# Performance work log

Measured on AMD Instinct MI355X. Metric: run time of the kernel, lower is better.

Reference implementation:

```python
import jax, jax.numpy as jnp
import numpy as np

C = 768; NH = 12; HD = C // NH; P = 16; IMG = 256; HS = IMG // P  # 16x16 patch grid
WIN = 7; HWP = WIN // 2  # half window (pad)
DEPTH = 12; MLP = 4 * C
B = 32; T = 1
OFFS = [(dh, dw) for dh in range(WIN) for dw in range(WIN)]


def ln(x, g, b, eps=1e-5):
    mu = jnp.mean(x, axis=-1, keepdims=True)
    var = jnp.mean((x - mu) ** 2, axis=-1, keepdims=True)
    return (x - mu) * jax.lax.rsqrt(var + eps) * g + b


def local_attn(x, qkv_w, proj_w, proj_b):
    # x: (B, N, C) with N = HS*HS (T=1); sliding-window attention, zero-padded keys
    Bc, N, _ = x.shape
    qkv = (x @ qkv_w.T).reshape(Bc, N, 3, NH, HD)
    q, k, v = [jnp.transpose(qkv[:, :, i], (0, 2, 1, 3)).reshape(Bc, NH, HS, HS, HD)
               for i in range(3)]
    scale = HD ** -0.5
    kp = jnp.pad(k, ((0, 0), (0, 0), (HWP, HWP), (HWP, HWP), (0, 0)))
    vp = jnp.pad(v, ((0, 0), (0, 0), (HWP, HWP), (HWP, HWP), (0, 0)))
    # per-offset logits; padded (zero) keys give logit 0, matching torch's zero-pad softmax
    scores = jnp.stack([
        jnp.einsum('bnhwd,bnhwd->bnhw', q, kp[:, :, dh:dh + HS, dw:dw + HS]) * scale
        for dh, dw in OFFS], axis=-1)  # (B, NH, HS, HS, 49)
    attn = jax.nn.softmax(scores, axis=-1)
    out = sum(attn[..., i, None] * vp[:, :, dh:dh + HS, dw:dw + HS]
              for i, (dh, dw) in enumerate(OFFS))  # (B, NH, HS, HS, HD)
    out = jnp.transpose(out, (0, 2, 3, 1, 4)).reshape(Bc, N, C)
    return out @ proj_w.T + proj_b


def global_attn(x, in_w, in_b, out_w, out_b):
    Bc, N, _ = x.shape
    qkv = x @ in_w.T + in_b
    q, k, v = jnp.split(qkv, 3, axis=-1)
    hds = lambda t: t.reshape(Bc, N, NH, HD).transpose(0, 2, 1, 3)
    q, k, v = hds(q), hds(k), hds(v)
    s = jnp.einsum('bnqd,bnkd->bnqk', q, k) * (HD ** -0.5)
    a = jax.nn.softmax(s, axis=-1)
    o = jnp.einsum('bnqk,bnkd->bnqd', a, v).transpose(0, 2, 1, 3).reshape(Bc, N, C)
    return o @ out_w.T + out_b


def setup_inputs() -> dict:
    key = jax.random.key(0)
    ks = iter(jax.random.split(key, 40))
    s = 0.02
    inp = {
        'x': jax.random.normal(next(ks), (B, T, 3, IMG, IMG), jnp.float32),
        'aspect_ratio': jax.random.uniform(next(ks), (B,), jnp.float32),
        'conv_w': jax.random.normal(next(ks), (C, 3, P, P), jnp.float32) * s,
        'conv_b': jnp.zeros((C,), jnp.float32),
        'pe_g': jnp.ones((C,), jnp.float32), 'pe_b': jnp.zeros((C,), jnp.float32),
        'ar_token': jax.random.normal(next(ks), (1, 1, C), jnp.float32) * s,
        'pos_embed': jax.random.normal(next(ks), (1, 100 * HS * HS + 1, C), jnp.float32) * s,
        'ln1_g': jnp.ones((DEPTH, C), jnp.float32), 'ln1_b': jnp.zeros((DEPTH, C), jnp.float32),
        'ln2_g': jnp.ones((DEPTH, C), jnp.float32), 'ln2_b': jnp.zeros((DEPTH, C), jnp.float32),
        'loc_qkv_w': jax.random.normal(next(ks), (6, 3 * C, C), jnp.float32) * s,
        'loc_proj_w': jax.random.normal(next(ks), (6, C, C), jnp.float32) * s,
        'loc_proj_b': jnp.zeros((6, C), jnp.float32),
        'glob_in_w': jax.random.normal(next(ks), (6, 3 * C, C), jnp.float32) * s,
        'glob_in_b': jnp.zeros((6, 3 * C), jnp.float32),
        'glob_out_w': jax.random.normal(next(ks), (6, C, C), jnp.float32) * s,
        'glob_out_b': jnp.zeros((6, C), jnp.float32),
        'mlp_w1': jax.random.normal(next(ks), (DEPTH, MLP, C), jnp.float32) * s,
        'mlp_b1': jnp.zeros((DEPTH, MLP), jnp.float32),
        'mlp_w2': jax.random.normal(next(ks), (DEPTH, C, MLP), jnp.float32) * s,
        'mlp_b2': jnp.zeros((DEPTH, C), jnp.float32),
        'fin_g': jnp.ones((C,), jnp.float32), 'fin_b': jnp.zeros((C,), jnp.float32),
    }
    return inp


def reference(x, aspect_ratio, conv_w, conv_b, pe_g, pe_b, ar_token, pos_embed,
              ln1_g, ln1_b, ln2_g, ln2_b,
              loc_qkv_w, loc_proj_w, loc_proj_b,
              glob_in_w, glob_in_b, glob_out_w, glob_out_b,
              mlp_w1, mlp_b1, mlp_w2, mlp_b2, fin_g, fin_b):
    Bc, Tc, Ci, Hi, Wi = x.shape
    # patch embed: non-overlapping conv == block reshape + einsum
    xf = x.reshape(Bc * Tc, Ci, HS, P, HS, P)
    patches = jnp.einsum('bchpwq,ecpq->bhwe', xf, conv_w) + conv_b
    patches = patches.reshape(Bc, Tc * HS * HS, C)
    patches = ln(patches, pe_g, pe_b)
    # aspect ratio token
    ar = ar_token * (1.0 + aspect_ratio[:, None, None] * 0.1)  # (B,1,C)
    h = jnp.concatenate([patches, ar], axis=1)
    h = h + pos_embed[:, :h.shape[1], :]
    for i in range(DEPTH):
        if i % 2 == 0:  # local attention block (AR token stripped, N == HS*HS+1)
            li = i // 2
            tok, art = h[:, :-1], h[:, -1:]
            tok = tok + local_attn(ln(tok, ln1_g[i], ln1_b[i]),
                                   loc_qkv_w[li], loc_proj_w[li], loc_proj_b[li])
            h = jnp.concatenate([tok, art], axis=1)
        else:
            gi = i // 2
            h = h + global_attn(ln(h, ln1_g[i], ln1_b[i]),
                                glob_in_w[gi], glob_in_b[gi], glob_out_w[gi], glob_out_b[gi])
        m = ln(h, ln2_g[i], ln2_b[i])
        m = jax.nn.gelu(m @ mlp_w1[i].T + mlp_b1[i], approximate=False)
        h = h + m @ mlp_w2[i].T + mlp_b2[i]
    return ln(h, fin_g, fin_b)
```

## Files before the change

### kernel.cpp

```cpp
#include <hip/hip_runtime.h>
#include <cmath>

#define NHEADS 12
#define NTOK   257
#define BATCH  32
#define ROWS   (BATCH*NTOK)
#define PROWS  (BATCH*256)
#define GTPAD  288

typedef __attribute__((ext_vector_type(8))) short short8;
typedef __attribute__((ext_vector_type(8))) unsigned short u16x8;
typedef __attribute__((ext_vector_type(4))) float f32x4;

__device__ __forceinline__ unsigned short f2bf(float f) {
    unsigned u = __float_as_uint(f);
    unsigned r = (u + 0x7FFFu + ((u >> 16) & 1u)) >> 16;
    return (unsigned short)r;
}
__device__ __forceinline__ float b2f(unsigned short us) {
    return __uint_as_float((unsigned)us << 16);
}
__device__ __forceinline__ void gload16(const void* g, void* l) {
    __builtin_amdgcn_global_load_lds(
        (const __attribute__((address_space(1))) void*)g,
        (__attribute__((address_space(3))) void*)l, 16, 0, 0);
}

template<bool BIAS, bool GELU, bool RES, bool SKIPAR, bool OUTBF>
__global__ __launch_bounds__(256) void gemm_bf16(
    const unsigned short* __restrict__ A, const unsigned short* __restrict__ W,
    const float* __restrict__ bias, void* __restrict__ outv,
    int M, int N, int K)
{
    __shared__ unsigned short As[2][128 * 64];
    __shared__ unsigned short Bs[2][128 * 64];
    const int tid = threadIdx.x;
    const int lane = tid & 63, wid = tid >> 6;
    const int wr = wid >> 1, wc = wid & 1;

    const int gx = gridDim.x;
    const int nwg = gx * gridDim.y;
    const int orig = blockIdx.y * gx + blockIdx.x;
    const int q8 = nwg >> 3, r8 = nwg & 7;
    const int xcd = orig & 7, lid = orig >> 3;
    const int wg = (xcd < r8 ? xcd * (q8 + 1) : r8 * (q8 + 1) + (xcd - r8) * q8) + lid;
    const int bn = (wg % gx) * 128;
    const int bm = (wg / gx) * 128;

    f32x4 acc[4][4];
    #pragma unroll
    for (int i = 0; i < 4; i++)
        #pragma unroll
        for (int j = 0; j < 4; j++) acc[i][j] = (f32x4)0.f;

    const int l15 = lane & 15;
    const int lg  = lane >> 4;
    const int sw  = l15 & 7;

    auto stage = [&](int buf, int k0) {
        #pragma unroll
        for (int it = 0; it < 4; it++) {
            int f = it * 256 + tid;
            int row = f >> 3;
            int g = (f & 7) ^ (row & 7);
            gload16(A + (size_t)(bm + row) * K + k0 + g * 8, &As[buf][f * 8]);
            gload16(W + (size_t)(bn + row) * K + k0 + g * 8, &Bs[buf][f * 8]);
        }
    };

    const int nt = K >> 6;
    stage(0, 0);

    int buf = 0;
    for (int t = 0; t < nt; t++) {
        if (t + 1 < nt) {
            stage(buf ^ 1, (t + 1) << 6);
            asm volatile("s_waitcnt vmcnt(8)\n\ts_barrier" ::: "memory");
        } else {
            asm volatile("s_waitcnt vmcnt(0)\n\ts_barrier" ::: "memory");
        }
        #pragma unroll
        for (int kk = 0; kk < 2; kk++) {
            short8 af[4], bf[4];
            #pragma unroll
            for (int i = 0; i < 4; i++) {
                int row = wr * 64 + i * 16 + l15;
                af[i] = *(const short8*)&As[buf][row * 64 + (((kk * 4 + lg) ^ sw)) * 8];
            }
            #pragma unroll
            for (int j = 0; j < 4; j++) {
                int row = wc * 64 + j * 16 + l15;
                bf[j] = *(const short8*)&Bs[buf][row * 64 + (((kk * 4 + lg) ^ sw)) * 8];
            }
            __builtin_amdgcn_s_setprio(1);
            #pragma unroll
            for (int i = 0; i < 4; i++)
                #pragma unroll
                for (int j = 0; j < 4; j++)
                    acc[i][j] = __builtin_amdgcn_mfma_f32_16x16x32_bf16(af[i], bf[j], acc[i][j], 0, 0, 0);
            __builtin_amdgcn_s_setprio(0);
        }
        asm volatile("s_barrier" ::: "memory");
        buf ^= 1;
    }

    float bcol[4];
    #pragma unroll
    for (int j = 0; j < 4; j++)
        bcol[j] = BIAS ? bias[bn + wc * 64 + j * 16 + l15] : 0.f;

    #pragma unroll
    for (int i = 0; i < 4; i++) {
        #pragma unroll
        for (int r = 0; r < 4; r++) {
            int row = bm + wr * 64 + i * 16 + lg * 4 + r;
            if (row >= M) continue;
            if (SKIPAR && (row % NTOK) == (NTOK - 1)) continue;
            #pragma unroll
            for (int j = 0; j < 4; j++) {
                int col = bn + wc * 64 + j * 16 + l15;
                float v = acc[i][j][r] + bcol[j];
                if (GELU) v = 0.5f * v * (1.0f + erff(v * 0.70710678118654752f));
                size_t idx = (size_t)row * N + col;
                if (OUTBF) {
                    ((unsigned short*)outv)[idx] = f2bf(v);
                } else {
                    float* o = (float*)outv;
                    if (RES) o[idx] += v; else o[idx] = v;
                }
            }
        }
    }
}

template<bool OUTBF>
__global__ __launch_bounds__(256) void ln_kernel(
    const float* __restrict__ in, void* __restrict__ outv,
    const float* __restrict__ g, const float* __restrict__ bparm, int rows)
{
    int gw = blockIdx.x * 4 + (threadIdx.x >> 6);
    int lane = threadIdx.x & 63;
    if (gw >= rows) return;
    const float* x = in + (size_t)gw * 768;
    float4 v[3];
    #pragma unroll
    for (int i = 0; i < 3; i++) v[i] = *(const float4*)(x + i * 256 + lane * 4);
    float s = 0.f;
    #pragma unroll
    for (int i = 0; i < 3; i++) s += v[i].x + v[i].y + v[i].z + v[i].w;
    #pragma unroll
    for (int off = 32; off >= 1; off >>= 1) s += __shfl_xor(s, off, 64);
    float mu = s * (1.f / 768.f);
    float q = 0.f;
    #pragma unroll
    for (int i = 0; i < 3; i++) {
        float dx = v[i].x - mu, dy = v[i].y - mu, dz = v[i].z - mu, dw = v[i].w - mu;
        q += dx * dx + dy * dy + dz * dz + dw * dw;
    }
    #pragma unroll
    for (int off = 32; off >= 1; off >>= 1) q += __shfl_xor(q, off, 64);
    float rstd = rsqrtf(q * (1.f / 768.f) + 1e-5f);
    #pragma unroll
    for (int i = 0; i < 3; i++) {
        float4 gg = *(const float4*)(g + i * 256 + lane * 4);
        float4 bb = *(const float4*)(bparm + i * 256 + lane * 4);
        float rx = (v[i].x - mu) * rstd * gg.x + bb.x;
        float ry = (v[i].y - mu) * rstd * gg.y + bb.y;
        float rz = (v[i].z - mu) * rstd * gg.z + bb.z;
        float rw = (v[i].w - mu) * rstd * gg.w + bb.w;
        if (OUTBF) {
            ushort4 u;
            u.x = f2bf(rx); u.y = f2bf(ry); u.z = f2bf(rz); u.w = f2bf(rw);
            *(ushort4*)((unsigned short*)outv + (size_t)gw * 768 + i * 256 + lane * 4) = u;
        } else {
            *(float4*)((float*)outv + (size_t)gw * 768 + i * 256 + lane * 4) =
                make_float4(rx, ry, rz, rw);
        }
    }
}

__global__ __launch_bounds__(256) void f2b_kernel(
    const float* __restrict__ in, unsigned short* __restrict__ out, int n4)
{
    int i = blockIdx.x * 256 + threadIdx.x;
    if (i >= n4) return;
    float4 v = ((const float4*)in)[i];
    ushort4 u;
    u.x = f2bf(v.x); u.y = f2bf(v.y); u.z = f2bf(v.z); u.w = f2bf(v.w);
    ((ushort4*)out)[i] = u;
}

__global__ __launch_bounds__(256) void gather_patches(
    const float* __restrict__ x, unsigned short* __restrict__ A)
{
    int row = blockIdx.x;
    int b = row >> 8;
    int pp = row & 255;
    int ph = pp >> 4, pw = pp & 15;
    const float* xb = x + (size_t)b * 196608;
    for (int e = threadIdx.x; e < 768; e += 256) {
        int c = e >> 8;
        int r = e & 255;
        int p = r >> 4, q = r & 15;
        A[(size_t)row * 768 + e] = f2bf(xb[(size_t)c * 65536 + (ph * 16 + p) * 256 + pw * 16 + q]);
    }
}

__global__ __launch_bounds__(256) void build_h_kernel(
    const unsigned short* __restrict__ lnp, const float* __restrict__ pos,
    const float* __restrict__ artok, const float* __restrict__ aspect,
    float* __restrict__ h)
{
    int row = blockIdx.x;
    int b = row / NTOK;
    int t = row - b * NTOK;
    float* hp = h + (size_t)row * 768;
    int e = threadIdx.x;
    if (t < 256) {
        const unsigned short* lp = lnp + ((size_t)b * 256 + t) * 768;
        const float* pp = pos + (size_t)t * 768;
        #pragma unroll
        for (int i = 0; i < 3; i++) { int c = e + i * 256; hp[c] = b2f(lp[c]) + pp[c]; }
    } else {
        float f = 1.0f + aspect[b] * 0.1f;
        const float* pp = pos + (size_t)256 * 768;
        #pragma unroll
        for (int i = 0; i < 3; i++) { int c = e + i * 256; hp[c] = artok[c] * f + pp[c]; }
    }
}

__global__ __launch_bounds__(256) void transpose_v(
    const unsigned short* __restrict__ qkv, unsigned short* __restrict__ vt)
{
    __shared__ unsigned short T[64][72];
    const int bh = blockIdx.x;
    const int b = bh / NHEADS, nh = bh % NHEADS;
    const unsigned short* vbase = qkv + (size_t)b * NTOK * 2304 + 1536 + nh * 64;
    unsigned short* obase = vt + (size_t)bh * 64 * GTPAD;
    const int tid = threadIdx.x;

    for (int t0 = 0; t0 < GTPAD; t0 += 64) {
        #pragma unroll
        for (int rnd = 0; rnd < 2; rnd++) {
            int tl = rnd * 32 + (tid >> 3);
            int d0 = (tid & 7) * 8;
            int tok = t0 + tl;
            u16x8 v;
            if (tok < NTOK) {
                v = *(const u16x8*)(vbase + (size_t)tok * 2304 + d0);
            } else {
                #pragma unroll
                for (int i = 0; i < 8; i++) v[i] = 0;
            }
            #pragma unroll
            for (int i = 0; i < 8; i++) T[d0 + i][tl] = v[i];
        }
        __syncthreads();
        int d = tid >> 2, ts = (tid & 3) * 16;
        if (t0 + ts < GTPAD) {
            u16x8 o0, o1;
            #pragma unroll
            for (int i = 0; i < 8; i++) { o0[i] = T[d][ts + i]; o1[i] = T[d][ts + 8 + i]; }
            *(u16x8*)(obase + (size_t)d * GTPAD + t0 + ts) = o0;
            *(u16x8*)(obase + (size_t)d * GTPAD + t0 + ts + 8) = o1;
        }
        __syncthreads();
    }
}

__global__ __launch_bounds__(256) void local_attn_mfma(
    const unsigned short* __restrict__ qkv, const unsigned short* __restrict__ vt,
    unsigned short* __restrict__ out)
{
    __shared__ unsigned short P[4][16 * 136];
    const int wid = threadIdx.x >> 6, lane = threadIdx.x & 63;
    const int gw = blockIdx.x * 4 + wid;
    const int bh = gw >> 4, h0 = gw & 15;
    const int b = bh / NHEADS, nh = bh % NHEADS;
    const int l15 = lane & 15, lg = lane >> 4;
    const unsigned short* base = qkv + (size_t)b * NTOK * 2304 + nh * 64;
    const unsigned short* vtb = vt + (size_t)bh * 64 * GTPAD;
    unsigned short* Pw = P[wid];

    const int qtok = h0 * 16 + l15;
    short8 qf0 = *(const short8*)(base + (size_t)qtok * 2304 + lg * 8);
    short8 qf1 = *(const short8*)(base + (size_t)qtok * 2304 + 32 + lg * 8);

    int r0 = h0 - 3; r0 = r0 < 0 ? 0 : (r0 > 8 ? 8 : r0);

    f32x4 s[8];
    #pragma unroll
    for (int i = 0; i < 8; i++) {
        const unsigned short* kr = base + (size_t)((r0 + i) * 16 + l15) * 2304 + 768;
        short8 kf0 = *(const short8*)(kr + lg * 8);
        short8 kf1 = *(const short8*)(kr + 32 + lg * 8);
        f32x4 z = (f32x4)0.f;
        z = __builtin_amdgcn_mfma_f32_16x16x32_bf16(kf0, qf0, z, 0, 0, 0);
        z = __builtin_amdgcn_mfma_f32_16x16x32_bf16(kf1, qf1, z, 0, 0, 0);
        s[i] = z;
    }

    const int vlo = l15 - 3 < 0 ? 0 : l15 - 3;
    const int vhi = l15 + 3 > 15 ? 15 : l15 + 3;
    const int rlo = h0 - 3 < 0 ? 0 : h0 - 3;
    const int rhi = h0 + 3 > 15 ? 15 : h0 + 3;
    const int n_oob = 49 - (rhi - rlo + 1) * (vhi - vlo + 1);
    float m = n_oob > 0 ? 0.f : -1e30f;
    float sv[32];
    #pragma unroll
    for (int i = 0; i < 8; i++) {
        int kh = r0 + i;
        bool rowok = (kh >= rlo) && (kh <= rhi);
        #pragma unroll
        for (int r = 0; r < 4; r++) {
            int kw = lg * 4 + r;
            bool ok = rowok && (kw >= vlo) && (kw <= vhi);
            float xx = ok ? s[i][r] * 0.125f : -1e30f;
            sv[i * 4 + r] = xx;
            m = fmaxf(m, xx);
        }
    }
    m = fmaxf(m, __shfl_xor(m, 16, 64));
    m = fmaxf(m, __shfl_xor(m, 32, 64));
    float tsum = 0.f;
    #pragma unroll
    for (int i = 0; i < 8; i++) {
        float p0 = __expf(sv[i * 4 + 0] - m);
        float p1 = __expf(sv[i * 4 + 1] - m);
        float p2 = __expf(sv[i * 4 + 2] - m);
        float p3 = __expf(sv[i * 4 + 3] - m);
        tsum += p0 + p1 + p2 + p3;
        unsigned u0 = (unsigned)f2bf(p0) | ((unsigned)f2bf(p1) << 16);
        unsigned u1 = (unsigned)f2bf(p2) | ((unsigned)f2bf(p3) << 16);
        *(uint2*)((char*)Pw + l15 * 272 + i * 32 + lg * 8) = make_uint2(u0, u1);
    }
    tsum += __shfl_xor(tsum, 16, 64);
    tsum += __shfl_xor(tsum, 32, 64);
    float denom = tsum + (float)n_oob * __expf(-m);
    __syncthreads();

    f32x4 acc[4];
    #pragma unroll
    for (int d = 0; d < 4; d++) acc[d] = (f32x4)0.f;
    #pragma unroll
    for (int kt = 0; kt < 128; kt += 32) {
        short8 pf = *(const short8*)((char*)Pw + l15 * 272 + kt * 2 + lg * 16);
        #pragma unroll
        for (int d = 0; d < 4; d++) {
            short8 vf = *(const short8*)(vtb + (size_t)(d * 16 + l15) * GTPAD + r0 * 16 + kt + lg * 8);
            acc[d] = __builtin_amdgcn_mfma_f32_16x16x32_bf16(vf, pf, acc[d], 0, 0, 0);
        }
    }

    float inv = 1.f / denom;
    unsigned short* op = out + ((size_t)b * NTOK + qtok) * 768 + nh * 64;
    #pragma unroll
    for (int d = 0; d < 4; d++) {
        ushort4 o;
        o.x = f2bf(acc[d][0] * inv);
        o.y = f2bf(acc[d][1] * inv);
        o.z = f2bf(acc[d][2] * inv);
        o.w = f2bf(acc[d][3] * inv);
        *(ushort4*)(op + d * 16 + lg * 4) = o;
    }
}

__global__ __launch_bounds__(64) void global_attn_mfma(
    const unsigned short* __restrict__ qkv, const unsigned short* __restrict__ vt,
    unsigned short* __restrict__ out)
{
    __shared__ uint4 Pbuf[80];
    unsigned short* P = (unsigned short*)Pbuf;
    const int blk = blockIdx.x;
    const int bh = blk / 17, qt = blk % 17;
    const int b = bh / NHEADS, nh = bh % NHEADS;
    const int lane = threadIdx.x;
    const int l15 = lane & 15, lg = lane >> 4;
    const unsigned short* base = qkv + (size_t)b * NTOK * 2304 + nh * 64;
    const unsigned short* vtb = vt + (size_t)bh * 64 * GTPAD;

    int qrow = qt * 16 + l15;
    const bool qvalid = qrow < NTOK;
    if (!qvalid) qrow = NTOK - 1;
    short8 qf[2];
    qf[0] = *(const short8*)(base + (size_t)qrow * 2304 + lg * 8);
    qf[1] = *(const short8*)(base + (size_t)qrow * 2304 + 32 + lg * 8);

    f32x4 acc[4];
    #pragma unroll
    for (int i = 0; i < 4; i++) acc[i] = (f32x4)0.f;
    float m = -1e30f, l = 0.f;

    for (int kt = 0; kt < GTPAD; kt += 32) {
        f32x4 s[2];
        #pragma unroll
        for (int hh = 0; hh < 2; hh++) {
            int krow = kt + hh * 16 + l15;
            if (krow > NTOK - 1) krow = NTOK - 1;
            short8 kf0 = *(const short8*)(base + (size_t)krow * 2304 + 768 + lg * 8);
            short8 kf1 = *(const short8*)(base + (size_t)krow * 2304 + 768 + 32 + lg * 8);
            f32x4 z = (f32x4)0.f;
            z = __builtin_amdgcn_mfma_f32_16x16x32_bf16(kf0, qf[0], z, 0, 0, 0);
            z = __builtin_amdgcn_mfma_f32_16x16x32_bf16(kf1, qf[1], z, 0, 0, 0);
            s[hh] = z;
        }
        float sv[8];
        float mt = -1e30f;
        #pragma unroll
        for (int hh = 0; hh < 2; hh++)
            #pragma unroll
            for (int r = 0; r < 4; r++) {
                int key = kt + hh * 16 + lg * 4 + r;
                float v = s[hh][r] * 0.125f;
                if (key >= NTOK) v = -1e30f;
                sv[hh * 4 + r] = v;
                mt = fmaxf(mt, v);
            }
        mt = fmaxf(mt, __shfl_xor(mt, 16, 64));
        mt = fmaxf(mt, __shfl_xor(mt, 32, 64));
        float mn = fmaxf(m, mt);
        float cf = __expf(m - mn);
        float tsum = 0.f;
        unsigned short pb[8];
        #pragma unroll
        for (int i = 0; i < 8; i++) {
            float p = __expf(sv[i] - mn);
            tsum += p;
            pb[i] = f2bf(p);
        }
        tsum += __shfl_xor(tsum, 16, 64);
        tsum += __shfl_xor(tsum, 32, 64);
        l = l * cf + tsum;
        m = mn;
        #pragma unroll
        for (int i = 0; i < 4; i++) acc[i] *= cf;

        unsigned u0 = (unsigned)pb[0] | ((unsigned)pb[1] << 16);
        unsigned u1 = (unsigned)pb[2] | ((unsigned)pb[3] << 16);
        unsigned u2 = (unsigned)pb[4] | ((unsigned)pb[5] << 16);
        unsigned u3 = (unsigned)pb[6] | ((unsigned)pb[7] << 16);
        *(uint2*)((char*)P + l15 * 80 + lg * 8)      = make_uint2(u0, u1);
        *(uint2*)((char*)P + l15 * 80 + 32 + lg * 8) = make_uint2(u2, u3);
        __syncthreads();
        short8 pf = *(const short8*)((char*)P + l15 * 80 + lg * 16);
        #pragma unroll
        for (int d = 0; d < 4; d++) {
            short8 vf = *(const short8*)(vtb + (size_t)(d * 16 + l15) * GTPAD + kt + lg * 8);
            acc[d] = __builtin_amdgcn_mfma_f32_16x16x32_bf16(vf, pf, acc[d], 0, 0, 0);
        }
        __syncthreads();
    }

    if (qvalid) {
        float inv = 1.f / l;
        unsigned short* op = out + ((size_t)b * NTOK + qrow) * 768 + nh * 64;
        #pragma unroll
        for (int d = 0; d < 4; d++) {
            ushort4 o;
            o.x = f2bf(acc[d][0] * inv);
            o.y = f2bf(acc[d][1] * inv);
            o.z = f2bf(acc[d][2] * inv);
            o.w = f2bf(acc[d][3] * inv);
            *(ushort4*)(op + d * 16 + lg * 4) = o;
        }
    }
}

extern "C" void kernel_launch(void* const* d_in, const int* in_sizes, int n_in,
                              void* d_out, int out_size, void* d_ws, size_t ws_size,
                              hipStream_t stream)
{
    const float* x       = (const float*)d_in[0];
    const float* aspect  = (const float*)d_in[1];
    const float* conv_w  = (const float*)d_in[2];
    const float* conv_b  = (const float*)d_in[3];
    const float* pe_g    = (const float*)d_in[4];
    const float* pe_b    = (const float*)d_in[5];
    const float* ar_tok  = (const float*)d_in[6];
    const float* pos     = (const float*)d_in[7];
    const float* ln1_g   = (const float*)d_in[8];
    const float* ln1_b   = (const float*)d_in[9];
    const float* ln2_g   = (const float*)d_in[10];
    const float* ln2_b   = (const float*)d_in[11];
    const float* loc_qkv_w  = (const float*)d_in[12];
    const float* loc_proj_w = (const float*)d_in[13];
    const float* loc_proj_b = (const float*)d_in[14];
    const float* glob_in_w  = (const float*)d_in[15];
    const float* glob_in_b  = (const float*)d_in[16];
    const float* glob_out_w = (const float*)d_in[17];
    const float* glob_out_b = (const float*)d_in[18];
    const float* mlp_w1  = (const float*)d_in[19];
    const float* mlp_b1  = (const float*)d_in[20];
    const float* mlp_w2  = (const float*)d_in[21];
    const float* mlp_b2  = (const float*)d_in[22];
    const float* fin_g   = (const float*)d_in[23];
    const float* fin_b   = (const float*)d_in[24];

    char* w = (char*)d_ws;
    float*          h     = (float*)w;
    unsigned short* lnb   = (unsigned short*)(w + 25264128);
    unsigned short* qkvb  = (unsigned short*)(w + 37896192);
    unsigned short* attnb = (unsigned short*)(w + 75792384);
    unsigned short* mlpb  = (unsigned short*)(w + 88424448);
    float*          pembf = (float*)mlpb;
    unsigned short* vtb   = mlpb;
    char* wp = w + 138952704;
    unsigned short* wconv  = (unsigned short*)wp;               wp += 1179648;
    unsigned short* wlqkv  = (unsigned short*)wp;               wp += 21233664;
    unsigned short* wlproj = (unsigned short*)wp;               wp += 7077888;
    unsigned short* wgin   = (unsigned short*)wp;               wp += 21233664;
    unsigned short* wgout  = (unsigned short*)wp;               wp += 7077888;
    unsigned short* wm1    = (unsigned short*)wp;               wp += 56623104;
    unsigned short* wm2    = (unsigned short*)wp;               wp += 56623104;

    auto cvt = [&](const float* src, unsigned short* dst, int n) {
        int n4 = n / 4;
        f2b_kernel<<<(n4 + 255) / 256, 256, 0, stream>>>(src, dst, n4);
    };
    cvt(conv_w,     wconv,  768 * 768);
    cvt(loc_qkv_w,  wlqkv,  6 * 2304 * 768);
    cvt(loc_proj_w, wlproj, 6 * 768 * 768);
    cvt(glob_in_w,  wgin,   6 * 2304 * 768);
    cvt(glob_out_w, wgout,  6 * 768 * 768);
    cvt(mlp_w1,     wm1,    12 * 3072 * 768);
    cvt(mlp_w2,     wm2,    12 * 768 * 3072);

    gather_patches<<<PROWS, 256, 0, stream>>>(x, qkvb);
    gemm_bf16<true, false, false, false, false><<<dim3(6, 64), 256, 0, stream>>>(
        qkvb, wconv, conv_b, pembf, PROWS, 768, 768);
    ln_kernel<true><<<PROWS / 4, 256, 0, stream>>>(pembf, attnb, pe_g, pe_b, PROWS);
    build_h_kernel<<<ROWS, 256, 0, stream>>>(attnb, pos, ar_tok, aspect, h);

    const int mt = (ROWS + 127) / 128;
    for (int i = 0; i < 12; i++) {
        int half = i / 2;
        ln_kernel<true><<<(ROWS + 3) / 4, 256, 0, stream>>>(h, lnb, ln1_g + i * 768, ln1_b + i * 768, ROWS);
        if ((i & 1) == 0) {
            gemm_bf16<false, false, false, false, true><<<dim3(18, mt), 256, 0, stream>>>(
                lnb, wlqkv + (size_t)half * 2304 * 768, nullptr, qkvb, ROWS, 2304, 768);
            transpose_v<<<BATCH * NHEADS, 256, 0, stream>>>(qkvb, vtb);
            local_attn_mfma<<<BATCH * NHEADS * 16 / 4, 256, 0, stream>>>(qkvb, vtb, attnb);
            gemm_bf16<true, false, true, true, false><<<dim3(6, mt), 256, 0, stream>>>(
                attnb, wlproj + (size_t)half * 768 * 768, loc_proj_b + half * 768, h, ROWS, 768, 768);
        } else {
            gemm_bf16<true, false, false, false, true><<<dim3(18, mt), 256, 0, stream>>>(
                lnb, wgin + (size_t)half * 2304 * 768, glob_in_b + half * 2304, qkvb, ROWS, 2304, 768);
            transpose_v<<<BATCH * NHEADS, 256, 0, stream>>>(qkvb, vtb);
            global_attn_mfma<<<BATCH * NHEADS * 17, 64, 0, stream>>>(qkvb, vtb, attnb);
            gemm_bf16<true, false, true, false, false><<<dim3(6, mt), 256, 0, stream>>>(
                attnb, wgout + (size_t)half * 768 * 768, glob_out_b + half * 768, h, ROWS, 768, 768);
        }
        ln_kernel<true><<<(ROWS + 3) / 4, 256, 0, stream>>>(h, lnb, ln2_g + i * 768, ln2_b + i * 768, ROWS);
        gemm_bf16<true, true, false, false, true><<<dim3(24, mt), 256, 0, stream>>>(
            lnb, wm1 + (size_t)i * 3072 * 768, mlp_b1 + i * 3072, mlpb, ROWS, 3072, 768);
        gemm_bf16<true, false, true, false, false><<<dim3(6, mt), 256, 0, stream>>>(
            mlpb, wm2 + (size_t)i * 768 * 3072, mlp_b2 + i * 768, h, ROWS, 768, 3072);
    }
    ln_kernel<false><<<(ROWS + 3) / 4, 256, 0, stream>>>(h, (float*)d_out, fin_g, fin_b, ROWS);
}
```

Baseline: 3.743 ms.

## Add 256x256-tile 512-thread bf16 GEMM for the MLP up-projection

Adds a new GEMM kernel with 256x256 output tiles, 8 waves per workgroup and double-buffered LDS staging, and uses it for the GELU MLP first GEMM. The larger tile raises arithmetic intensity per LDS and global load, cutting load traffic on the largest GEMM. In exchange it uses about 128KB of LDS and 128 accumulator registers per lane, and leaves only 396 workgroups, which can cause tail imbalance; the last M tile also reads rows further past M. The existing 128-tile GEMM is also rewritten to use plain __syncthreads with setprio removed, and it carries a dead leftover expression.

```diff
diff --git a/kernel.cpp b/kernel.cpp
--- a/kernel.cpp
+++ b/kernel.cpp
@@ -62,9 +62,114 @@
         for (int it = 0; it < 4; it++) {
             int f = it * 256 + tid;
             int row = f >> 3;
-            int g = (f & 7) ^ (row & 7);
-            gload16(A + (size_t)(bm + row) * K + k0 + g * 8, &As[buf][f * 8]);
-            gload16(W + (size_t)(bn + row) * K + k0 + g * 8, &Bs[buf][f * 8]);
+            int g = (f & 3 * 2 + (f & 7) - (f & 7)) ; (void)g;
+            int gc = (f & 7) ^ (row & 7);
+            gload16(A + (size_t)(bm + row) * K + k0 + gc * 8, &As[buf][f * 8]);
+            gload16(W + (size_t)(bn + row) * K + k0 + gc * 8, &Bs[buf][f * 8]);
+        }
+    };
+
+    const int nt = K >> 6;
+    stage(0, 0);
+    __syncthreads();
+
+    int buf = 0;
+    for (int t = 0; t < nt; t++) {
+        if (t + 1 < nt) stage(buf ^ 1, (t + 1) << 6);
+        #pragma unroll
+        for (int kk = 0; kk < 2; kk++) {
+            short8 af[4], bf[4];
+            #pragma unroll
+            for (int i = 0; i < 4; i++) {
+                int row = wr * 64 + i * 16 + l15;
+                af[i] = *(const short8*)&As[buf][row * 64 + (((kk * 4 + lg) ^ sw)) * 8];
+            }
+            #pragma unroll
+            for (int j = 0; j < 4; j++) {
+                int row = wc * 64 + j * 16 + l15;
+                bf[j] = *(const short8*)&Bs[buf][row * 64 + (((kk * 4 + lg) ^ sw)) * 8];
+            }
+            #pragma unroll
+            for (int i = 0; i < 4; i++)
+                #pragma unroll
+                for (int j = 0; j < 4; j++)
+                    acc[i][j] = __builtin_amdgcn_mfma_f32_16x16x32_bf16(af[i], bf[j], acc[i][j], 0, 0, 0);
+        }
+        __syncthreads();
+        buf ^= 1;
+    }
+
+    float bcol[4];
+    #pragma unroll
+    for (int j = 0; j < 4; j++)
+        bcol[j] = BIAS ? bias[bn + wc * 64 + j * 16 + l15] : 0.f;
+
+    #pragma unroll
+    for (int i = 0; i < 4; i++) {
+        #pragma unroll
+        for (int r = 0; r < 4; r++) {
+            int row = bm + wr * 64 + i * 16 + lg * 4 + r;
+            if (row >= M) continue;
+            if (SKIPAR && (row % NTOK) == (NTOK - 1)) continue;
+            #pragma unroll
+            for (int j = 0; j < 4; j++) {
+                int col = bn + wc * 64 + j * 16 + l15;
+                float v = acc[i][j][r] + bcol[j];
+                if (GELU) v = 0.5f * v * (1.0f + erff(v * 0.70710678118654752f));
+                size_t idx = (size_t)row * N + col;
+                if (OUTBF) {
+                    ((unsigned short*)outv)[idx] = f2bf(v);
+                } else {
+                    float* o = (float*)outv;
+                    if (RES) o[idx] += v; else o[idx] = v;
+                }
+            }
+        }
+    }
+}
+
+template<bool BIAS, bool GELU, bool RES, bool SKIPAR, bool OUTBF>
+__global__ __launch_bounds__(512) void gemm256(
+    const unsigned short* __restrict__ A, const unsigned short* __restrict__ W,
+    const float* __restrict__ bias, void* __restrict__ outv,
+    int M, int N, int K)
+{
+    __shared__ unsigned short As[2][256 * 64];
+    __shared__ unsigned short Bs[2][256 * 64];
+    const int tid = threadIdx.x;
+    const int lane = tid & 63, wid = tid >> 6;
+    const int wr = wid >> 2, wc = wid & 3;
+
+    const int gx = gridDim.x;
+    const int nwg = gx * gridDim.y;
+    const int orig = blockIdx.y * gx + blockIdx.x;
+    const int q8 = nwg >> 3, r8 = nwg & 7;
+    const int xcd = orig & 7, lid = orig >> 3;
+    const int wg = (xcd < r8 ? xcd * (q8 + 1) : r8 * (q8 + 1) + (xcd - r8) * q8) + lid;
+    const int bn = (wg % gx) * 256;
+    const int bm = (wg / gx) * 256;
+
+    f32x4 acc[8][4];
+    #pragma unroll
+    for (int i = 0; i < 8; i++)
+        #pragma unroll
+        for (int j = 0; j < 4; j++) acc[i][j] = (f32x4)0.f;
+
+    const int l15 = lane & 15;
+    const int lg  = lane >> 4;
+    const int sw  = l15 & 7;
+
+    const int r0 = tid >> 3;
+    const int gsrc = (tid & 7) ^ (r0 & 7);
+    const int wub = (tid & 448) * 8;
+
+    auto stage = [&](int buf, int k0) {
+        #pragma unroll
+        for (int it = 0; it < 4; it++) {
+            gload16(A + (size_t)(bm + it * 64 + r0) * K + k0 + gsrc * 8,
+                    &As[buf][it * 4096 + wub]);
+            gload16(W + (size_t)(bn + it * 64 + r0) * K + k0 + gsrc * 8,
+                    &Bs[buf][it * 4096 + wub]);
         }
     };
 
@@ -81,10 +186,10 @@
         }
         #pragma unroll
         for (int kk = 0; kk < 2; kk++) {
-            short8 af[4], bf[4];
-            #pragma unroll
-            for (int i = 0; i < 4; i++) {
-                int row = wr * 64 + i * 16 + l15;
+            short8 af[8], bf[4];
+            #pragma unroll
+            for (int i = 0; i < 8; i++) {
+                int row = wr * 128 + i * 16 + l15;
                 af[i] = *(const short8*)&As[buf][row * 64 + (((kk * 4 + lg) ^ sw)) * 8];
             }
             #pragma unroll
@@ -94,7 +199,7 @@
             }
             __builtin_amdgcn_s_setprio(1);
             #pragma unroll
-            for (int i = 0; i < 4; i++)
+            for (int i = 0; i < 8; i++)
                 #pragma unroll
                 for (int j = 0; j < 4; j++)
                     acc[i][j] = __builtin_amdgcn_mfma_f32_16x16x32_bf16(af[i], bf[j], acc[i][j], 0, 0, 0);
@@ -110,10 +215,10 @@
         bcol[j] = BIAS ? bias[bn + wc * 64 + j * 16 + l15] : 0.f;
 
     #pragma unroll
-    for (int i = 0; i < 4; i++) {
+    for (int i = 0; i < 8; i++) {
         #pragma unroll
         for (int r = 0; r < 4; r++) {
-            int row = bm + wr * 64 + i * 16 + lg * 4 + r;
+            int row = bm + wr * 128 + i * 16 + lg * 4 + r;
             if (row >= M) continue;
             if (SKIPAR && (row % NTOK) == (NTOK - 1)) continue;
             #pragma unroll
@@ -532,6 +637,7 @@
     build_h_kernel<<<ROWS, 256, 0, stream>>>(attnb, pos, ar_tok, aspect, h);
 
     const int mt = (ROWS + 127) / 128;
+    const int mt2 = (ROWS + 255) / 256;
     for (int i = 0; i < 12; i++) {
         int half = i / 2;
         ln_kernel<true><<<(ROWS + 3) / 4, 256, 0, stream>>>(h, lnb, ln1_g + i * 768, ln1_b + i * 768, ROWS);
@@ -551,7 +657,7 @@
                 attnb, wgout + (size_t)half * 768 * 768, glob_out_b + half * 768, h, ROWS, 768, 768);
         }
         ln_kernel<true><<<(ROWS + 3) / 4, 256, 0, stream>>>(h, lnb, ln2_g + i * 768, ln2_b + i * 768, ROWS);
-        gemm_bf16<true, true, false, false, true><<<dim3(24, mt), 256, 0, stream>>>(
+        gemm256<true, true, false, false, true><<<dim3(12, mt2), 512, 0, stream>>>(
             lnb, wm1 + (size_t)i * 3072 * 768, mlp_b1 + i * 3072, mlpb, ROWS, 3072, 768);
         gemm_bf16<true, false, true, false, false><<<dim3(6, mt), 256, 0, stream>>>(
             mlpb, wm2 + (size_t)i * 768 * 3072, mlp_b2 + i * 768, h, ROWS, 768, 3072);
```

Result: no change. 3.726 ms (-0.5%).
